# Kernel optimization log

Hardware: AMD Instinct MI355X
Metric: run time of the kernel (lower is better)

The kernel has to match this reference:

```python
import jax, jax.numpy as jnp
import numpy as np

B, T, C, H = 4, 2048, 768, 768  # batch, seq, embed_size, embed_size_h


def setup_inputs() -> dict:
    key = jax.random.key(0)
    ks = jax.random.split(key, 7)
    s = 1.0 / np.sqrt(C)  # torch Linear default-ish init scale
    return {
        "x": jax.random.normal(ks[0], (B, T, C), jnp.float32),
        "Wq": jax.random.normal(ks[1], (C, H), jnp.float32) * s,
        "bq": jnp.zeros((H,), jnp.float32),
        "Wk": jax.random.normal(ks[2], (C, H), jnp.float32) * s,
        "bk": jnp.zeros((H,), jnp.float32),
        "Wv": jax.random.normal(ks[3], (C, H), jnp.float32) * s,
        "bv": jnp.zeros((H,), jnp.float32),
    }


def reference(x, Wq, bq, Wk, bk, Wv, bv):
    # q,k,v: [B,T,H]
    q = x @ Wq + bq
    k = x @ Wk + bk
    v = x @ Wv + bv
    scale = jnp.asarray(H, x.dtype) ** -0.5
    # full [B,T,T] score matrix, as the original module does
    qk = jnp.einsum("btd,bsd->bts", q, k) * scale
    tril = jnp.tril(jnp.ones((T, T), x.dtype))
    qk = qk * tril
    # original quirk: masked_fill on exact zeros (covers upper triangle)
    qk = jnp.where(qk == 0, -jnp.inf, qk)
    attn = jax.nn.softmax(qk, axis=-1)  # [B,T,T]
    # note: in the source, dropout is applied to a dead value; output uses softmax directly
    return attn @ v  # [B,T,H]
```

## Files before the change

kernel.cpp:

```cpp
#include <hip/hip_runtime.h>
#include <math.h>


#define BB 4
#define TT 2048
#define CC 768

typedef __bf16 bf16_t;
typedef __bf16 bf16x8 __attribute__((ext_vector_type(8)));
typedef _Float16 half8 __attribute__((ext_vector_type(8)));
typedef float f32x4 __attribute__((ext_vector_type(4)));

__device__ __forceinline__ void async_load16(void* lds, const void* g) {
  __builtin_amdgcn_global_load_lds(
      (const __attribute__((address_space(1))) void*)g,
      (__attribute__((address_space(3))) void*)lds, 16, 0, 0);
}

__device__ __forceinline__ void stage_tile(const bf16_t* __restrict__ g0,
                                           int ld, bf16_t* lds, int t) {
  int w = t >> 6, l = t & 63;
#pragma unroll
  for (int i = 0; i < 2; ++i) {
    int c = i * 256 + w * 64 + l;
    int row = c >> 2;
    int p = c & 3;
    int q = p ^ (row & 3);
    async_load16(lds + i * 2048 + w * 512,
                 g0 + row * ld + q * 8);
  }
}

__device__ __forceinline__ bf16x8 read_frag(const bf16_t* lds, int r, int q) {
  int p = q ^ (r & 3);
  return *(const bf16x8*)(lds + r * 32 + p * 8);
}

__device__ __forceinline__ void mfma_tile(const bf16_t* Ab, const bf16_t* Bb,
                                          int wr, int wc, int l,
                                          f32x4 acc[4][4]) {
  bf16x8 af[4], bfr[4];
  int q = l >> 4;
#pragma unroll
  for (int i = 0; i < 4; ++i) {
    af[i] = read_frag(Ab, wr + i * 16 + (l & 15), q);
    bfr[i] = read_frag(Bb, wc + i * 16 + (l & 15), q);
  }
#pragma unroll
  for (int mi = 0; mi < 4; ++mi)
#pragma unroll
    for (int ni = 0; ni < 4; ++ni)
      acc[mi][ni] = __builtin_amdgcn_mfma_f32_16x16x32_bf16(
          af[mi], bfr[ni], acc[mi][ni], 0, 0, 0);
}

__device__ __forceinline__ void gemm_core(const bf16_t* __restrict__ A, int lda,
                                          const bf16_t* __restrict__ B, int ldb,
                                          int kTiles, bf16_t* As0, bf16_t* As1,
                                          bf16_t* Bs0, bf16_t* Bs1,
                                          f32x4 acc[4][4]) {
  int t = threadIdx.x;
  int l = t & 63;
  int w = t >> 6;
  int wr = (w >> 1) * 64;
  int wc = (w & 1) * 64;

  stage_tile(A, lda, As0, t);
  stage_tile(B, ldb, Bs0, t);

  for (int kt = 0; kt < kTiles; kt += 2) {
    __syncthreads();
    stage_tile(A + (kt + 1) * 32, lda, As1, t);
    stage_tile(B + (kt + 1) * 32, ldb, Bs1, t);
    mfma_tile(As0, Bs0, wr, wc, l, acc);
    __syncthreads();
    if (kt + 2 < kTiles) {
      stage_tile(A + (kt + 2) * 32, lda, As0, t);
      stage_tile(B + (kt + 2) * 32, ldb, Bs0, t);
    }
    mfma_tile(As1, Bs1, wr, wc, l, acc);
  }
}


__global__ __launch_bounds__(256) void cast_x_kernel(
    const float* __restrict__ x, bf16_t* __restrict__ xbf) {
  int i = blockIdx.x * 256 + threadIdx.x;
  const float4* xin = (const float4*)x;
  float4 a = xin[i * 2];
  float4 b = xin[i * 2 + 1];
  bf16_t tmp[8];
  tmp[0] = (bf16_t)a.x; tmp[1] = (bf16_t)a.y;
  tmp[2] = (bf16_t)a.z; tmp[3] = (bf16_t)a.w;
  tmp[4] = (bf16_t)b.x; tmp[5] = (bf16_t)b.y;
  tmp[6] = (bf16_t)b.z; tmp[7] = (bf16_t)b.w;
  *(uint4*)(xbf + (size_t)i * 8) = *(const uint4*)tmp;
}

__global__ __launch_bounds__(256) void transpose_w_kernel(
    const float* __restrict__ Wq, const float* __restrict__ Wk,
    const float* __restrict__ Wv, bf16_t* __restrict__ wt) {
  int z = blockIdx.z;
  const float* W = (z == 0) ? Wq : (z == 1) ? Wk : Wv;
  bf16_t* out = wt + (size_t)z * CC * CC;
  __shared__ float tile[32][33];
  int tx = threadIdx.x;
  int ty = threadIdx.y;
  int n0 = blockIdx.x * 32;
  int c0 = blockIdx.y * 32;
#pragma unroll
  for (int k = 0; k < 4; ++k)
    tile[ty + k * 8][tx] = W[(size_t)(c0 + ty + k * 8) * CC + n0 + tx];
  __syncthreads();
#pragma unroll
  for (int k = 0; k < 4; ++k)
    out[(size_t)(n0 + ty + k * 8) * CC + c0 + tx] =
        (bf16_t)tile[tx][ty + k * 8];
}

__global__ __launch_bounds__(256) void qkv_gemm_kernel(
    const bf16_t* __restrict__ xbf, const bf16_t* __restrict__ wt,
    const float* __restrict__ bq, const float* __restrict__ bk,
    const float* __restrict__ bv, bf16_t* __restrict__ qb,
    bf16_t* __restrict__ kb, bf16_t* __restrict__ vt) {
  __shared__ bf16_t As0[4096], As1[4096], Bs0[4096], Bs1[4096];
  int n0 = blockIdx.x * 128;
  int m0 = blockIdx.y * 128;
  int z = blockIdx.z;

  f32x4 acc[4][4];
#pragma unroll
  for (int i = 0; i < 4; ++i)
#pragma unroll
    for (int j = 0; j < 4; ++j) acc[i][j] = (f32x4){0.f, 0.f, 0.f, 0.f};

  const bf16_t* A = xbf + (size_t)m0 * CC;
  const bf16_t* B = wt + (size_t)z * CC * CC + (size_t)n0 * CC;
  gemm_core(A, CC, B, CC, CC / 32, As0, As1, Bs0, Bs1, acc);

  int l = threadIdx.x & 63, w = threadIdx.x >> 6;
  int wr = (w >> 1) * 64, wc = (w & 1) * 64;
  const float* bias = (z == 0) ? bq : (z == 1) ? bk : bv;
  float scale = (z == 0) ? rsqrtf((float)CC) : 1.0f;

#pragma unroll
  for (int mi = 0; mi < 4; ++mi) {
#pragma unroll
    for (int ni = 0; ni < 4; ++ni) {
      int col = n0 + wc + ni * 16 + (l & 15);
      int rbase = m0 + wr + mi * 16 + (l >> 4) * 4;
      float bcol = bias[col];
#pragma unroll
      for (int r = 0; r < 4; ++r) {
        int m = rbase + r;
        float v = (acc[mi][ni][r] + bcol) * scale;
        bf16_t h = (bf16_t)v;
        if (z == 0) {
          qb[(size_t)m * CC + col] = h;
        } else if (z == 1) {
          kb[(size_t)m * CC + col] = h;
        } else {
          int b = m >> 11, tt = m & (TT - 1);
          vt[((size_t)b * CC + col) * TT + tt] = h;
        }
      }
    }
  }
}

__global__ __launch_bounds__(256) void s_gemm_kernel(
    const bf16_t* __restrict__ qb, const bf16_t* __restrict__ kb,
    _Float16* __restrict__ S) {
  int tj = blockIdx.x, ti = blockIdx.y, b = blockIdx.z;
  if (tj > ti) return;
  __shared__ bf16_t As0[4096], As1[4096], Bs0[4096], Bs1[4096];
  int m0 = ti * 128, n0 = tj * 128;

  f32x4 acc[4][4];
#pragma unroll
  for (int i = 0; i < 4; ++i)
#pragma unroll
    for (int j = 0; j < 4; ++j) acc[i][j] = (f32x4){0.f, 0.f, 0.f, 0.f};

  const bf16_t* A = qb + ((size_t)b * TT + m0) * CC;
  const bf16_t* B = kb + ((size_t)b * TT + n0) * CC;
  gemm_core(A, CC, B, CC, CC / 32, As0, As1, Bs0, Bs1, acc);

  _Float16* Sb = S + (size_t)b * TT * TT;
  int l = threadIdx.x & 63, w = threadIdx.x >> 6;
  int wr = (w >> 1) * 64, wc = (w & 1) * 64;
#pragma unroll
  for (int mi = 0; mi < 4; ++mi) {
#pragma unroll
    for (int ni = 0; ni < 4; ++ni) {
      int j = n0 + wc + ni * 16 + (l & 15);
      int ibase = m0 + wr + mi * 16 + (l >> 4) * 4;
#pragma unroll
      for (int r = 0; r < 4; ++r) {
        int i = ibase + r;
        float v = acc[mi][ni][r];
        if (j > i || v == 0.0f) v = -INFINITY;
        Sb[(size_t)i * TT + j] = (_Float16)v;
      }
    }
  }
}

__global__ __launch_bounds__(256) void rowstat_kernel(
    const _Float16* __restrict__ S, bf16_t* __restrict__ P) {
  int row = blockIdx.x & (TT - 1);
  int b = blockIdx.x >> 11;
  const _Float16* s = S + ((size_t)b * TT + row) * TT;
  bf16_t* p = P + ((size_t)b * TT + row) * TT;
  int pe = ((row >> 7) + 1) << 7;
  int j = threadIdx.x * 8;
  bool live = j < pe;

  float f[8];
  if (live) {
    half8 h = *(const half8*)(s + j);
#pragma unroll
    for (int k = 0; k < 8; ++k) f[k] = (float)h[k];
  } else {
#pragma unroll
    for (int k = 0; k < 8; ++k) f[k] = -INFINITY;
  }

  float m = f[0];
#pragma unroll
  for (int k = 1; k < 8; ++k) m = fmaxf(m, f[k]);
#pragma unroll
  for (int off = 32; off > 0; off >>= 1) m = fmaxf(m, __shfl_xor(m, off));
  __shared__ float redm[4];
  int w = threadIdx.x >> 6, l = threadIdx.x & 63;
  if (l == 0) redm[w] = m;
  __syncthreads();
  m = fmaxf(fmaxf(redm[0], redm[1]), fmaxf(redm[2], redm[3]));

  float e[8];
  float sum = 0.f;
#pragma unroll
  for (int k = 0; k < 8; ++k) {
    e[k] = __expf(f[k] - m);
    sum += e[k];
  }
#pragma unroll
  for (int off = 32; off > 0; off >>= 1) sum += __shfl_xor(sum, off);
  __shared__ float reds[4];
  if (l == 0) reds[w] = sum;
  __syncthreads();
  float inv = 1.0f / (reds[0] + reds[1] + reds[2] + reds[3]);

  if (live) {
    bf16x8 o;
#pragma unroll
    for (int k = 0; k < 8; ++k) o[k] = (bf16_t)(e[k] * inv);
    *(bf16x8*)(p + j) = o;
  }
}

__global__ __launch_bounds__(256) void o_gemm_kernel(
    const bf16_t* __restrict__ P, const bf16_t* __restrict__ vt,
    float* __restrict__ out) {
  int nj = blockIdx.x;
  int ti = (int)gridDim.y - 1 - (int)blockIdx.y;
  int b = blockIdx.z;
  __shared__ bf16_t As0[4096], As1[4096], Bs0[4096], Bs1[4096];
  int m0 = ti * 128, n0 = nj * 128;

  f32x4 acc[4][4];
#pragma unroll
  for (int i = 0; i < 4; ++i)
#pragma unroll
    for (int j = 0; j < 4; ++j) acc[i][j] = (f32x4){0.f, 0.f, 0.f, 0.f};

  const bf16_t* A = P + ((size_t)b * TT + m0) * TT;
  const bf16_t* B = vt + ((size_t)b * CC + n0) * TT;
  gemm_core(A, TT, B, TT, (ti + 1) * 4, As0, As1, Bs0, Bs1, acc);

  float* Ob = out + (size_t)b * TT * CC;
  int l = threadIdx.x & 63, w = threadIdx.x >> 6;
  int wr = (w >> 1) * 64, wc = (w & 1) * 64;
#pragma unroll
  for (int mi = 0; mi < 4; ++mi) {
#pragma unroll
    for (int ni = 0; ni < 4; ++ni) {
      int col = n0 + wc + ni * 16 + (l & 15);
      int ibase = m0 + wr + mi * 16 + (l >> 4) * 4;
#pragma unroll
      for (int r = 0; r < 4; ++r)
        Ob[(size_t)(ibase + r) * CC + col] = acc[mi][ni][r];
    }
  }
}

extern "C" void kernel_launch(void* const* d_in, const int* in_sizes, int n_in,
                              void* d_out, int out_size, void* d_ws,
                              size_t ws_size, hipStream_t stream) {
  const float* x = (const float*)d_in[0];
  const float* Wq = (const float*)d_in[1];
  const float* bq = (const float*)d_in[2];
  const float* Wk = (const float*)d_in[3];
  const float* bk = (const float*)d_in[4];
  const float* Wv = (const float*)d_in[5];
  const float* bv = (const float*)d_in[6];
  float* out = (float*)d_out;

  char* ws = (char*)d_ws;
  size_t off = 0;
  auto carve = [&](size_t bytes) -> char* {
    char* p = ws + off;
    off += (bytes + 255) & ~(size_t)255;
    return p;
  };
  const size_t M = (size_t)BB * TT;
  bf16_t* xbf = (bf16_t*)carve(M * CC * 2);
  bf16_t* wt  = (bf16_t*)carve(3ull * CC * CC * 2);
  bf16_t* qb  = (bf16_t*)carve(M * CC * 2);
  bf16_t* kb  = (bf16_t*)carve(M * CC * 2);
  bf16_t* vt  = (bf16_t*)carve(M * CC * 2);
  _Float16* S = (_Float16*)carve((size_t)BB * TT * TT * 2);
  bf16_t* P   = (bf16_t*)carve((size_t)BB * TT * TT * 2);
  (void)off; (void)ws_size;

  cast_x_kernel<<<(M * CC / 8 + 255) / 256, 256, 0, stream>>>(x, xbf);
  transpose_w_kernel<<<dim3(CC / 32, CC / 32, 3), dim3(32, 8, 1), 0, stream>>>(
      Wq, Wk, Wv, wt);
  qkv_gemm_kernel<<<dim3(CC / 128, M / 128, 3), 256, 0, stream>>>(
      xbf, wt, bq, bk, bv, qb, kb, vt);
  s_gemm_kernel<<<dim3(TT / 128, TT / 128, BB), 256, 0, stream>>>(qb, kb, S);
  rowstat_kernel<<<BB * TT, 256, 0, stream>>>(S, P);
  o_gemm_kernel<<<dim3(CC / 128, TT / 128, BB), 256, 0, stream>>>(P, vt, out);
}
```

Measured before the change: 236.7 us.

## Replace double-buffered LDS pipeline with single-buffer load-then-compute loop

```diff
diff --git a/kernel.cpp b/kernel.cpp
--- a/kernel.cpp
+++ b/kernel.cpp
@@ -36,28 +36,9 @@
   return *(const bf16x8*)(lds + r * 32 + p * 8);
 }
 
-__device__ __forceinline__ void mfma_tile(const bf16_t* Ab, const bf16_t* Bb,
-                                          int wr, int wc, int l,
-                                          f32x4 acc[4][4]) {
-  bf16x8 af[4], bfr[4];
-  int q = l >> 4;
-#pragma unroll
-  for (int i = 0; i < 4; ++i) {
-    af[i] = read_frag(Ab, wr + i * 16 + (l & 15), q);
-    bfr[i] = read_frag(Bb, wc + i * 16 + (l & 15), q);
-  }
-#pragma unroll
-  for (int mi = 0; mi < 4; ++mi)
-#pragma unroll
-    for (int ni = 0; ni < 4; ++ni)
-      acc[mi][ni] = __builtin_amdgcn_mfma_f32_16x16x32_bf16(
-          af[mi], bfr[ni], acc[mi][ni], 0, 0, 0);
-}
-
 __device__ __forceinline__ void gemm_core(const bf16_t* __restrict__ A, int lda,
                                           const bf16_t* __restrict__ B, int ldb,
-                                          int kTiles, bf16_t* As0, bf16_t* As1,
-                                          bf16_t* Bs0, bf16_t* Bs1,
+                                          int kTiles, bf16_t* As, bf16_t* Bs,
                                           f32x4 acc[4][4]) {
   int t = threadIdx.x;
   int l = t & 63;
@@ -65,20 +46,25 @@
   int wr = (w >> 1) * 64;
   int wc = (w & 1) * 64;
 
-  stage_tile(A, lda, As0, t);
-  stage_tile(B, ldb, Bs0, t);
-
-  for (int kt = 0; kt < kTiles; kt += 2) {
+  for (int kt = 0; kt < kTiles; ++kt) {
     __syncthreads();
-    stage_tile(A + (kt + 1) * 32, lda, As1, t);
-    stage_tile(B + (kt + 1) * 32, ldb, Bs1, t);
-    mfma_tile(As0, Bs0, wr, wc, l, acc);
+    stage_tile(A + kt * 32, lda, As, t);
+    stage_tile(B + kt * 32, ldb, Bs, t);
     __syncthreads();
-    if (kt + 2 < kTiles) {
-      stage_tile(A + (kt + 2) * 32, lda, As0, t);
-      stage_tile(B + (kt + 2) * 32, ldb, Bs0, t);
+
+    bf16x8 af[4], bfr[4];
+    int q = l >> 4;
+#pragma unroll
+    for (int i = 0; i < 4; ++i) {
+      af[i] = read_frag(As, wr + i * 16 + (l & 15), q);
+      bfr[i] = read_frag(Bs, wc + i * 16 + (l & 15), q);
     }
-    mfma_tile(As1, Bs1, wr, wc, l, acc);
+#pragma unroll
+    for (int mi = 0; mi < 4; ++mi)
+#pragma unroll
+      for (int ni = 0; ni < 4; ++ni)
+        acc[mi][ni] = __builtin_amdgcn_mfma_f32_16x16x32_bf16(
+            af[mi], bfr[ni], acc[mi][ni], 0, 0, 0);
   }
 }
 
@@ -123,7 +109,8 @@
     const float* __restrict__ bq, const float* __restrict__ bk,
     const float* __restrict__ bv, bf16_t* __restrict__ qb,
     bf16_t* __restrict__ kb, bf16_t* __restrict__ vt) {
-  __shared__ bf16_t As0[4096], As1[4096], Bs0[4096], Bs1[4096];
+  __shared__ bf16_t As[128 * 32];
+  __shared__ bf16_t Bs[128 * 32];
   int n0 = blockIdx.x * 128;
   int m0 = blockIdx.y * 128;
   int z = blockIdx.z;
@@ -136,7 +123,7 @@
 
   const bf16_t* A = xbf + (size_t)m0 * CC;
   const bf16_t* B = wt + (size_t)z * CC * CC + (size_t)n0 * CC;
-  gemm_core(A, CC, B, CC, CC / 32, As0, As1, Bs0, Bs1, acc);
+  gemm_core(A, CC, B, CC, CC / 32, As, Bs, acc);
 
   int l = threadIdx.x & 63, w = threadIdx.x >> 6;
   int wr = (w >> 1) * 64, wc = (w & 1) * 64;
@@ -173,7 +160,8 @@
     _Float16* __restrict__ S) {
   int tj = blockIdx.x, ti = blockIdx.y, b = blockIdx.z;
   if (tj > ti) return;
-  __shared__ bf16_t As0[4096], As1[4096], Bs0[4096], Bs1[4096];
+  __shared__ bf16_t As[128 * 32];
+  __shared__ bf16_t Bs[128 * 32];
   int m0 = ti * 128, n0 = tj * 128;
 
   f32x4 acc[4][4];
@@ -184,7 +172,7 @@
 
   const bf16_t* A = qb + ((size_t)b * TT + m0) * CC;
   const bf16_t* B = kb + ((size_t)b * TT + n0) * CC;
-  gemm_core(A, CC, B, CC, CC / 32, As0, As1, Bs0, Bs1, acc);
+  gemm_core(A, CC, B, CC, CC / 32, As, Bs, acc);
 
   _Float16* Sb = S + (size_t)b * TT * TT;
   int l = threadIdx.x & 63, w = threadIdx.x >> 6;
@@ -265,7 +253,8 @@
   int nj = blockIdx.x;
   int ti = (int)gridDim.y - 1 - (int)blockIdx.y;
   int b = blockIdx.z;
-  __shared__ bf16_t As0[4096], As1[4096], Bs0[4096], Bs1[4096];
+  __shared__ bf16_t As[128 * 32];
+  __shared__ bf16_t Bs[128 * 32];
   int m0 = ti * 128, n0 = nj * 128;
 
   f32x4 acc[4][4];
@@ -276,7 +265,7 @@
 
   const bf16_t* A = P + ((size_t)b * TT + m0) * TT;
   const bf16_t* B = vt + ((size_t)b * CC + n0) * TT;
-  gemm_core(A, TT, B, TT, (ti + 1) * 4, As0, As1, Bs0, Bs1, acc);
+  gemm_core(A, TT, B, TT, (ti + 1) * 4, As, Bs, acc);
 
   float* Ob = out + (size_t)b * TT * CC;
   int l = threadIdx.x & 63, w = threadIdx.x >> 6;
```

Result: slower. 253.4 us (+7.0%).
